# Kernel optimization log

Hardware: AMD Instinct MI355X
Metric: run time of the kernel (lower is better)

Reference implementation:

```python
import jax, jax.numpy as jnp
import numpy as np

B, S, D, H = 2, 2048, 1024, 16
HD = D // H  # 64


def setup_inputs() -> dict:
    key = jax.random.key(0)
    ks = jax.random.split(key, 10)
    s = 1.0 / np.sqrt(D)
    X = jax.random.normal(ks[0], (B, S, D), dtype=jnp.float32)
    # pad the last 256 key positions (nonzero = ignore); causal rows still
    # attend to earlier unpadded keys so no all-masked rows.
    kpm = jnp.broadcast_to((jnp.arange(S) >= S - 256).astype(jnp.int32), (B, S))
    return {
        "X": X,
        "key_padding_mask": kpm,
        "Wq": jax.random.uniform(ks[1], (D, D), jnp.float32, -s, s),
        "bq": jax.random.uniform(ks[2], (D,), jnp.float32, -s, s),
        "Wk": jax.random.uniform(ks[3], (D, D), jnp.float32, -s, s),
        "bk": jax.random.uniform(ks[4], (D,), jnp.float32, -s, s),
        "Wv": jax.random.uniform(ks[5], (D, D), jnp.float32, -s, s),
        "bv": jax.random.uniform(ks[6], (D,), jnp.float32, -s, s),
        "Wo": jax.random.uniform(ks[7], (D, D), jnp.float32, -s, s),
        "bo": jax.random.uniform(ks[8], (D,), jnp.float32, -s, s),
    }


def _mha(X, kpm, Wq, bq, Wk, bk, Wv, bv, Wo, bo):
    b, s, d = X.shape
    def heads(t):  # (b,s,d) -> (b,H,s,hd)
        return t.reshape(b, s, H, HD).transpose(0, 2, 1, 3)
    Q = heads(X @ Wq.T + bq)
    K = heads(X @ Wk.T + bk)
    V = heads(X @ Wv.T + bv)
    scores = jnp.einsum('bhqd,bhkd->bhqk', Q, K) / jnp.sqrt(jnp.float32(HD))
    causal = jnp.triu(jnp.ones((s, s), dtype=bool), k=1)  # True above diag
    scores = jnp.where(causal[None, None], -jnp.inf, scores)
    scores = jnp.where(kpm[:, None, None, :] != 0, -jnp.inf, scores)
    A = jax.nn.softmax(scores, axis=-1)
    out = jnp.einsum('bhqk,bhkd->bhqd', A, V)  # (b,H,s,hd)
    out = out.transpose(0, 2, 1, 3).reshape(b, s, d)
    return out @ Wo.T + bo


def reference(X, key_padding_mask, Wq, bq, Wk, bk, Wv, bv, Wo, bo):
    return _mha(X, key_padding_mask, Wq, bq, Wk, bk, Wv, bv, Wo, bo)
```

## Files before the change

kernel.cpp:

```cpp
#include <hip/hip_runtime.h>
#include <math.h>

#define DEV __device__ __forceinline__

typedef __attribute__((ext_vector_type(4))) float f32x4;
typedef __attribute__((ext_vector_type(8))) __bf16 bf16x8;

static constexpr int Bc = 2, Sc = 2048, Dc = 1024, Hc = 16, HDc = 64;
static constexpr int LDQ = 3 * Dc;
static constexpr float SCL = 0.125f * 1.44269504f;

DEV unsigned short f2b(float f) {
  union { float f; unsigned int u; } c; c.f = f;
  unsigned int u = c.u;
  unsigned int r = (u + 0x7fffu + ((u >> 16) & 1u)) >> 16;
  return (unsigned short)r;
}

DEV void async16(const void* g, void* l) {
  __builtin_amdgcn_global_load_lds(
      (__attribute__((address_space(1))) void*)(void*)g,
      (__attribute__((address_space(3))) void*)l, 16, 0, 0);
}

DEV int swz(int r, int c) { return r * 64 + (c ^ ((r & 7) << 3)); }

__global__ void cvt_all(const float* __restrict__ X, const float* __restrict__ Wq,
                        const float* __restrict__ Wk, const float* __restrict__ Wv,
                        const float* __restrict__ Wo,
                        unsigned short* __restrict__ Xb,
                        unsigned short* __restrict__ Wb) {
  const int i = blockIdx.x * blockDim.x + threadIdx.x;
  const float* src;
  unsigned short* dst;
  int o;
  if (i < (1 << 20)) {
    src = X; o = i; dst = Xb;
  } else {
    const int wi = i - (1 << 20);
    const int m = wi >> 18;
    src = m == 0 ? Wq : m == 1 ? Wk : m == 2 ? Wv : Wo;
    o = wi & ((1 << 18) - 1);
    dst = Wb + (size_t)m * (Dc * Dc);
  }
  const float4 v = reinterpret_cast<const float4*>(src)[o];
  ushort4 u;
  u.x = f2b(v.x); u.y = f2b(v.y); u.z = f2b(v.z); u.w = f2b(v.w);
  reinterpret_cast<ushort4*>(dst)[o] = u;
}

template <typename OUT>
__global__ __launch_bounds__(256, 3) void gemm_bt(
    const unsigned short* __restrict__ A, const unsigned short* __restrict__ Bm,
    const float* __restrict__ b0, const float* __restrict__ b1,
    const float* __restrict__ b2, OUT* __restrict__ C, int M, int K, int ldc) {
  __shared__ unsigned short As[128 * 64];
  __shared__ unsigned short Bs[128 * 64];
  const int tid = threadIdx.x;
  const int wave = tid >> 6, lane = tid & 63;
  const int wr = wave >> 1, wc = wave & 1;
  const int cpx = gridDim.x >> 3;
  const int swzid = (blockIdx.x & 7) * cpx + (blockIdx.x >> 3);
  const int row0 = (swzid & 31) * 128, col0 = (swzid >> 5) * 128;
  const int srow = lane >> 3, scol = (lane & 7) * 8;

  f32x4 acc[4][4];
#pragma unroll
  for (int m = 0; m < 4; ++m)
#pragma unroll
    for (int n = 0; n < 4; ++n) acc[m][n] = {0.f, 0.f, 0.f, 0.f};

  for (int k0 = 0; k0 < K; k0 += 64) {
    __syncthreads();
#pragma unroll
    for (int c = 0; c < 4; ++c) {
      const int rr = (wave * 4 + c) * 8 + srow;
      async16(A + (size_t)(row0 + rr) * K + k0 + scol,
              (char*)As + (wave * 4 + c) * 1024);
      async16(Bm + (size_t)(col0 + rr) * K + k0 + scol,
              (char*)Bs + (wave * 4 + c) * 1024);
    }
    __syncthreads();
#pragma unroll
    for (int ks = 0; ks < 2; ++ks) {
      const int kk = ks * 32 + (lane >> 4) * 8;
      bf16x8 af[4], bfr[4];
#pragma unroll
      for (int m = 0; m < 4; ++m)
        af[m] = *reinterpret_cast<const bf16x8*>(
            &As[(wr * 64 + m * 16 + (lane & 15)) * 64 + kk]);
#pragma unroll
      for (int n = 0; n < 4; ++n)
        bfr[n] = *reinterpret_cast<const bf16x8*>(
            &Bs[(wc * 64 + n * 16 + (lane & 15)) * 64 + kk]);
#pragma unroll
      for (int m = 0; m < 4; ++m)
#pragma unroll
        for (int n = 0; n < 4; ++n)
          acc[m][n] = __builtin_amdgcn_mfma_f32_16x16x32_bf16(af[m], bfr[n],
                                                              acc[m][n], 0, 0, 0);
    }
  }
  const int r4 = (lane >> 4) * 4, cl = lane & 15;
#pragma unroll
  for (int n = 0; n < 4; ++n) {
    const int gc = col0 + wc * 64 + n * 16 + cl;
    const float* bp = gc < Dc ? b0 : (gc < 2 * Dc ? b1 : b2);
    const float bv = bp[gc & (Dc - 1)];
#pragma unroll
    for (int m = 0; m < 4; ++m) {
#pragma unroll
      for (int j = 0; j < 4; ++j) {
        const int gr = row0 + wr * 64 + m * 16 + r4 + j;
        const float v = acc[m][n][j] + bv;
        if constexpr (sizeof(OUT) == 4)
          C[(size_t)gr * ldc + gc] = v;
        else
          C[(size_t)gr * ldc + gc] = (OUT)f2b(v);
      }
    }
  }
}

__global__ __launch_bounds__(256, 4) void attn_fwd(
    const __bf16* __restrict__ Qg, const __bf16* __restrict__ Kg,
    const __bf16* __restrict__ Vg, const int* __restrict__ kpm,
    __bf16* __restrict__ Og) {
  __shared__ __bf16 QP[64 * 64];
  __shared__ __bf16 Ks[2][64 * 64];
  __shared__ __bf16 Vt[2][64 * 64];

  const int L = blockIdx.x;
  const int s = L >> 8, c = L & 255;
  const int u = c >> 5, bh = c & 31;
  const int qb = s * 8 + ((s & 1) ? (7 - u) : u);

  const int b = bh >> 4, h = bh & 15;
  const int q0 = qb * 64;
  const int tid = threadIdx.x, wave = tid >> 6, lane = tid & 63;
  const size_t base = (size_t)b * Sc * LDQ + (size_t)h * HDc;
  const int srow = lane >> 3;
  const int scol = 8 * ((lane & 7) ^ srow);
  const int hi = lane >> 4, cl = lane & 15, r4 = hi * 4;

  const int vk2 = (tid & 31) * 2, vd8 = (tid >> 5) * 8;
  const __bf16* vbase = Vg + base + (size_t)vk2 * LDQ + vd8;
  const int* mbase = kpm + b * Sc;

  union VV { uint4 q; unsigned short u[8]; };

#pragma unroll
  for (int cc = 0; cc < 2; ++cc) {
    const int rr = (wave * 2 + cc) * 8 + srow;
    async16(Qg + base + (size_t)(q0 + rr) * LDQ + scol,
            (char*)QP + (wave * 2 + cc) * 1024);
    async16(Kg + base + (size_t)rr * LDQ + scol,
            (char*)Ks[0] + (wave * 2 + cc) * 1024);
  }
  VV v0, v1;
  v0.q = *reinterpret_cast<const uint4*>(vbase);
  v1.q = *reinterpret_cast<const uint4*>(vbase + LDQ);
  int mki[4];
#pragma unroll
  for (int n = 0; n < 4; ++n) mki[n] = mbase[n * 16 + cl];
  {
    unsigned int* V32 = reinterpret_cast<unsigned int*>(Vt[0]);
#pragma unroll
    for (int i = 0; i < 8; ++i) {
      const int row = vd8 + i;
      V32[row * 32 + ((tid & 31) ^ ((row & 7) << 2))] =
          (unsigned int)v0.u[i] | ((unsigned int)v1.u[i] << 16);
    }
  }
  __syncthreads();

  bf16x8 qf[2];
#pragma unroll
  for (int ks = 0; ks < 2; ++ks)
    qf[ks] = *reinterpret_cast<const bf16x8*>(
        &QP[swz(wave * 16 + cl, ks * 32 + hi * 8)]);
  __bf16* Ps = QP + wave * 1024;

  bf16x8 ones;
#pragma unroll
  for (int i = 0; i < 8; ++i) ones[i] = (__bf16)1.0f;

  f32x4 o[4], lacc;
  float m_[4];
#pragma unroll
  for (int n = 0; n < 4; ++n) o[n] = {0.f, 0.f, 0.f, 0.f};
  lacc = {0.f, 0.f, 0.f, 0.f};
#pragma unroll
  for (int j = 0; j < 4; ++j) m_[j] = -1e30f;

  int pb = 0;
  for (int kb = 0; kb <= qb; ++kb) {
    const bool diag = (kb == qb);
    VV n0, n1;
    int nmk[4];
    if (!diag) {
      const int k1 = (kb + 1) * 64;
#pragma unroll
      for (int cc = 0; cc < 2; ++cc) {
        const int rr = (wave * 2 + cc) * 8 + srow;
        async16(Kg + base + (size_t)(k1 + rr) * LDQ + scol,
                (char*)Ks[pb ^ 1] + (wave * 2 + cc) * 1024);
      }
      n0.q = *reinterpret_cast<const uint4*>(vbase + (size_t)k1 * LDQ);
      n1.q = *reinterpret_cast<const uint4*>(vbase + (size_t)(k1 + 1) * LDQ);
#pragma unroll
      for (int n = 0; n < 4; ++n) nmk[n] = mbase[k1 + n * 16 + cl];
    }

    f32x4 sa[4];
#pragma unroll
    for (int n = 0; n < 4; ++n) sa[n] = {0.f, 0.f, 0.f, 0.f};
    __builtin_amdgcn_s_setprio(1);
#pragma unroll
    for (int ks = 0; ks < 2; ++ks) {
      const int kk = ks * 32 + hi * 8;
#pragma unroll
      for (int n = 0; n < 4; ++n) {
        if (!(diag && n > wave)) {
          const bf16x8 kf = *reinterpret_cast<const bf16x8*>(
              &Ks[pb][swz(n * 16 + cl, kk)]);
          sa[n] = __builtin_amdgcn_mfma_f32_16x16x32_bf16(qf[ks], kf, sa[n],
                                                          0, 0, 0);
        }
      }
    }
    __builtin_amdgcn_s_setprio(0);
    float pm[4] = {-1e30f, -1e30f, -1e30f, -1e30f};
#pragma unroll
    for (int n = 0; n < 4; ++n) {
      const float mf = mki[n] ? -1e30f : 0.0f;
#pragma unroll
      for (int j = 0; j < 4; ++j) {
        float s2 = fmaf(sa[n][j], SCL, mf);
        if (diag && (kb * 64 + n * 16 + cl > q0 + wave * 16 + r4 + j))
          s2 = -1e30f;
        sa[n][j] = s2;
        pm[j] = fmaxf(pm[j], s2);
      }
    }
    const bool ok = (pm[0] - m_[0] <= 8.f) && (pm[1] - m_[1] <= 8.f) &&
                    (pm[2] - m_[2] <= 8.f) && (pm[3] - m_[3] <= 8.f);
    if (!__all(ok)) {
#pragma unroll
      for (int off = 1; off < 16; off <<= 1)
#pragma unroll
        for (int j = 0; j < 4; ++j)
          pm[j] = fmaxf(pm[j], __shfl_xor(pm[j], off, 64));
#pragma unroll
      for (int j = 0; j < 4; ++j) {
        const float mn = fmaxf(m_[j], pm[j]);
        const float sc = __builtin_amdgcn_exp2f(m_[j] - mn);
        m_[j] = mn;
        lacc[j] *= sc;
#pragma unroll
        for (int n = 0; n < 4; ++n) o[n][j] *= sc;
      }
    }
#pragma unroll
    for (int n = 0; n < 4; ++n)
#pragma unroll
      for (int j = 0; j < 4; ++j) {
        const float p = __builtin_amdgcn_exp2f(sa[n][j] - m_[j]);
        Ps[swz(r4 + j, n * 16 + cl)] = (__bf16)p;
      }
    __builtin_amdgcn_s_setprio(1);
#pragma unroll
    for (int ks = 0; ks < 2; ++ks) {
      const int kk = ks * 32 + hi * 8;
      const bf16x8 pf = *reinterpret_cast<const bf16x8*>(&Ps[swz(cl, kk)]);
#pragma unroll
      for (int n = 0; n < 4; ++n) {
        const bf16x8 vf = *reinterpret_cast<const bf16x8*>(
            &Vt[pb][swz(n * 16 + cl, kk)]);
        o[n] = __builtin_amdgcn_mfma_f32_16x16x32_bf16(pf, vf, o[n], 0, 0, 0);
      }
      lacc = __builtin_amdgcn_mfma_f32_16x16x32_bf16(pf, ones, lacc, 0, 0, 0);
    }
    __builtin_amdgcn_s_setprio(0);
    if (!diag) {
      unsigned int* V32 = reinterpret_cast<unsigned int*>(Vt[pb ^ 1]);
#pragma unroll
      for (int i = 0; i < 8; ++i) {
        const int row = vd8 + i;
        V32[row * 32 + ((tid & 31) ^ ((row & 7) << 2))] =
            (unsigned int)n0.u[i] | ((unsigned int)n1.u[i] << 16);
      }
#pragma unroll
      for (int n = 0; n < 4; ++n) mki[n] = nmk[n];
    }
    __syncthreads();
    pb ^= 1;
  }

#pragma unroll
  for (int j = 0; j < 4; ++j) {
    const float inv = 1.f / lacc[j];
#pragma unroll
    for (int n = 0; n < 4; ++n)
      Og[(size_t)(b * Sc + q0 + wave * 16 + r4 + j) * Dc + h * HDc + n * 16 +
         cl] = (__bf16)(o[n][j] * inv);
  }
}

extern "C" void kernel_launch(void* const* d_in, const int* in_sizes, int n_in,
                              void* d_out, int out_size, void* d_ws,
                              size_t ws_size, hipStream_t stream) {
  const float* X = (const float*)d_in[0];
  const int* kpm = (const int*)d_in[1];
  const float* Wq = (const float*)d_in[2];
  const float* bq = (const float*)d_in[3];
  const float* Wk = (const float*)d_in[4];
  const float* bk = (const float*)d_in[5];
  const float* Wv = (const float*)d_in[6];
  const float* bv = (const float*)d_in[7];
  const float* Wo = (const float*)d_in[8];
  const float* bo = (const float*)d_in[9];
  float* out = (float*)d_out;

  char* w = (char*)d_ws;
  unsigned short* Xb = (unsigned short*)(w);
  unsigned short* Wqkvb = (unsigned short*)(w + (8u << 20));
  unsigned short* Wob = (unsigned short*)(w + (14u << 20));
  unsigned short* QKVb = (unsigned short*)(w + (16u << 20));
  unsigned short* Ab = (unsigned short*)(w + (40u << 20));

  const int MD = Bc * Sc;
  cvt_all<<<dim3(8192), 256, 0, stream>>>(X, Wq, Wk, Wv, Wo, Xb, Wqkvb);

  gemm_bt<unsigned short><<<dim3(32 * 24), 256, 0, stream>>>(
      Xb, Wqkvb, bq, bk, bv, QKVb, MD, Dc, LDQ);

  attn_fwd<<<dim3(1024), 256, 0, stream>>>(
      (const __bf16*)QKVb, (const __bf16*)QKVb + Dc,
      (const __bf16*)QKVb + 2 * Dc, kpm, (__bf16*)Ab);

  gemm_bt<float><<<dim3(32 * 8), 256, 0, stream>>>(
      Ab, Wob, bo, bo, bo, out, MD, Dc, Dc);
}
```

Measured before the change: 120.4 us.

## Load Q and K fragments directly from global memory into registers, dropping LDS staging

Q fragments are now read directly from global memory into registers instead of being staged through shared memory. K fragments for each key block are also loaded straight from global memory into registers each iteration, replacing the double-buffered async LDS copy. This cuts shared memory use (which may raise occupancy) and removes LDS round trips. In exchange, the K loads are no longer prefetched one block ahead, so global-memory latency sits directly in front of the MFMA chain, and each wave re-reads K from global/L2 redundantly.

```diff
diff --git a/kernel.cpp b/kernel.cpp
--- a/kernel.cpp
+++ b/kernel.cpp
@@ -126,8 +126,7 @@
     const __bf16* __restrict__ Qg, const __bf16* __restrict__ Kg,
     const __bf16* __restrict__ Vg, const int* __restrict__ kpm,
     __bf16* __restrict__ Og) {
-  __shared__ __bf16 QP[64 * 64];
-  __shared__ __bf16 Ks[2][64 * 64];
+  __shared__ __bf16 Ps_all[4 * 16 * 64];
   __shared__ __bf16 Vt[2][64 * 64];
 
   const int L = blockIdx.x;
@@ -139,8 +138,6 @@
   const int q0 = qb * 64;
   const int tid = threadIdx.x, wave = tid >> 6, lane = tid & 63;
   const size_t base = (size_t)b * Sc * LDQ + (size_t)h * HDc;
-  const int srow = lane >> 3;
-  const int scol = 8 * ((lane & 7) ^ srow);
   const int hi = lane >> 4, cl = lane & 15, r4 = hi * 4;
 
   const int vk2 = (tid & 31) * 2, vd8 = (tid >> 5) * 8;
@@ -149,14 +146,14 @@
 
   union VV { uint4 q; unsigned short u[8]; };
 
-#pragma unroll
-  for (int cc = 0; cc < 2; ++cc) {
-    const int rr = (wave * 2 + cc) * 8 + srow;
-    async16(Qg + base + (size_t)(q0 + rr) * LDQ + scol,
-            (char*)QP + (wave * 2 + cc) * 1024);
-    async16(Kg + base + (size_t)rr * LDQ + scol,
-            (char*)Ks[0] + (wave * 2 + cc) * 1024);
-  }
+  const __bf16* qrow =
+      Qg + base + (size_t)(q0 + wave * 16 + cl) * LDQ + hi * 8;
+  bf16x8 qf[2];
+  qf[0] = *reinterpret_cast<const bf16x8*>(qrow);
+  qf[1] = *reinterpret_cast<const bf16x8*>(qrow + 32);
+
+  const __bf16* kfb = Kg + base + (size_t)cl * LDQ + hi * 8;
+
   VV v0, v1;
   v0.q = *reinterpret_cast<const uint4*>(vbase);
   v1.q = *reinterpret_cast<const uint4*>(vbase + LDQ);
@@ -172,14 +169,7 @@
           (unsigned int)v0.u[i] | ((unsigned int)v1.u[i] << 16);
     }
   }
-  __syncthreads();
-
-  bf16x8 qf[2];
-#pragma unroll
-  for (int ks = 0; ks < 2; ++ks)
-    qf[ks] = *reinterpret_cast<const bf16x8*>(
-        &QP[swz(wave * 16 + cl, ks * 32 + hi * 8)]);
-  __bf16* Ps = QP + wave * 1024;
+  __bf16* Ps = Ps_all + wave * 1024;
 
   bf16x8 ones;
 #pragma unroll
@@ -192,6 +182,8 @@
   lacc = {0.f, 0.f, 0.f, 0.f};
 #pragma unroll
   for (int j = 0; j < 4; ++j) m_[j] = -1e30f;
+
+  __syncthreads();
 
   int pb = 0;
   for (int kb = 0; kb <= qb; ++kb) {
@@ -200,32 +192,31 @@
     int nmk[4];
     if (!diag) {
       const int k1 = (kb + 1) * 64;
-#pragma unroll
-      for (int cc = 0; cc < 2; ++cc) {
-        const int rr = (wave * 2 + cc) * 8 + srow;
-        async16(Kg + base + (size_t)(k1 + rr) * LDQ + scol,
-                (char*)Ks[pb ^ 1] + (wave * 2 + cc) * 1024);
-      }
       n0.q = *reinterpret_cast<const uint4*>(vbase + (size_t)k1 * LDQ);
       n1.q = *reinterpret_cast<const uint4*>(vbase + (size_t)(k1 + 1) * LDQ);
 #pragma unroll
       for (int n = 0; n < 4; ++n) nmk[n] = mbase[k1 + n * 16 + cl];
     }
 
+    bf16x8 kf[2][4];
+#pragma unroll
+    for (int ks = 0; ks < 2; ++ks)
+#pragma unroll
+      for (int n = 0; n < 4; ++n)
+        kf[ks][n] = *reinterpret_cast<const bf16x8*>(
+            kfb + (size_t)(kb * 64 + n * 16) * LDQ + ks * 32);
+
     f32x4 sa[4];
 #pragma unroll
     for (int n = 0; n < 4; ++n) sa[n] = {0.f, 0.f, 0.f, 0.f};
     __builtin_amdgcn_s_setprio(1);
 #pragma unroll
     for (int ks = 0; ks < 2; ++ks) {
-      const int kk = ks * 32 + hi * 8;
 #pragma unroll
       for (int n = 0; n < 4; ++n) {
         if (!(diag && n > wave)) {
-          const bf16x8 kf = *reinterpret_cast<const bf16x8*>(
-              &Ks[pb][swz(n * 16 + cl, kk)]);
-          sa[n] = __builtin_amdgcn_mfma_f32_16x16x32_bf16(qf[ks], kf, sa[n],
-                                                          0, 0, 0);
+          sa[n] = __builtin_amdgcn_mfma_f32_16x16x32_bf16(qf[ks], kf[ks][n],
+                                                          sa[n], 0, 0, 0);
         }
       }
     }
```

Result: slower. 168.9 us, median of 2 (+40.3%).
